# Kernel tuning notes

Measured on AMD Instinct MI355X. Metric: run time of the kernel, lower is better.

Reference implementation:

```python
import jax, jax.numpy as jnp
import numpy as np

B, S, C, D, P = 32, 720, 2048, 256, 96
LATENT_DIMS = [512, 128, 32]  # enc_in // 4 ** k, e_layers=3
NL = 3
ALPHA = 0.1
EPS = 1e-5


def _ln(x, g, b, eps=1e-5):
    m = jnp.mean(x, axis=-1, keepdims=True)
    v = jnp.var(x, axis=-1, keepdims=True)
    return (x - m) * jax.lax.rsqrt(v + eps) * g + b


def _cov_loss(skips, lam=ALPHA, eps=EPS):
    total = jnp.zeros((), dtype=jnp.float32)
    for x in skips[1:]:
        b, c, d = x.shape
        xr = x.reshape(b * c, d)
        xc = (xr - jnp.mean(xr, axis=0, keepdims=True)) / (jnp.std(xr, axis=0, ddof=1, keepdims=True) + eps)
        cov = xc.T @ xc / (b * c - 1) + eps * jnp.eye(d, dtype=x.dtype)
        total = total - jnp.linalg.slogdet(cov)[1] / d
    return lam * total / (len(skips) - 1)


def setup_inputs() -> dict:
    key = jax.random.key(0)
    ks = jax.random.split(key, 16)
    w = lambda k, shp: (jax.random.normal(k, shp, dtype=jnp.float32) * 0.02)
    inp = {
        'x_enc': jax.random.normal(ks[0], (B, S, C), dtype=jnp.float32),
        'x_mark_enc': jnp.zeros((B, S, 4), dtype=jnp.float32),
        'x_dec': jnp.zeros((B, P, C), dtype=jnp.float32),
        'x_mark_dec': jnp.zeros((B, P, 4), dtype=jnp.float32),
        'in_w': w(ks[1], (S, D)), 'in_b': jnp.zeros((D,), jnp.float32),
        'lq0': jax.random.normal(ks[2], (LATENT_DIMS[0], D), dtype=jnp.float32),
        'lq1': jax.random.normal(ks[3], (LATENT_DIMS[1], D), dtype=jnp.float32),
        'lq2': jax.random.normal(ks[4], (LATENT_DIMS[2], D), dtype=jnp.float32),
        'down_w': w(ks[5], (NL, 4, D, D)), 'down_b': jnp.zeros((NL, 4, D), jnp.float32),
        'down_ln': jnp.stack([jnp.ones((NL, D)), jnp.zeros((NL, D))], axis=1).astype(jnp.float32),
        'pred_w': w(ks[6], (D, D)), 'pred_b': jnp.zeros((D,), jnp.float32),
        'up_w': w(ks[7], (NL, 4, D, D)), 'up_b': jnp.zeros((NL, 4, D), jnp.float32),
        'up_ln': jnp.stack([jnp.ones((NL, D)), jnp.zeros((NL, D))], axis=1).astype(jnp.float32),
        'out_w': w(ks[8], (D, P)), 'out_b': jnp.zeros((P,), jnp.float32),
    }
    return inp


def _forward(x_enc, in_w, in_b, lqs, down_w, down_b, down_ln,
             pred_w, pred_b, up_w, up_b, up_ln, out_w, out_b):
    # instance norm over time
    means = jnp.mean(x_enc, axis=1, keepdims=True)            # [B,1,C]
    xc = x_enc - means
    stdev = jnp.sqrt(jnp.var(xc, axis=1, keepdims=True) + 1e-5)
    xn = xc / stdev
    # transpose + Linear(seq_len -> d_model): [B,C,D]
    h = jnp.einsum('bsc,sd->bcd', xn, in_w) + in_b

    scale = 1.0 / jnp.sqrt(jnp.asarray(D, dtype=h.dtype))
    skips = [h]
    x = h
    for i in range(NL):
        Wq, Wk, Wv, Wo = down_w[i]
        bq, bk, bv, bo = down_b[i]
        q = lqs[i] @ Wq + bq                                  # [Lq,D] shared over batch
        k = x @ Wk + bk                                       # [B,L,D]
        v = x @ Wv + bv
        attn = jax.nn.softmax(jnp.einsum('qd,bld->bql', q, k) * scale, axis=-1)
        o = jnp.einsum('bql,bld->bqd', attn, v) @ Wo + bo
        x = _ln(o, down_ln[i, 0], down_ln[i, 1])
        skips.append(x)

    cov = _cov_loss(skips)

    x = x @ pred_w + pred_b                                   # bottom [B,32,D]
    queries = skips[::-1][1:]                                 # [128-skip, 512-skip, base]
    for i, qin in enumerate(queries):
        Wq, Wk, Wv, Wo = up_w[i]
        bq, bk, bv, bo = up_b[i]
        q = qin @ Wq + bq                                     # [B,Lq,D]
        k = x @ Wk + bk                                       # [B,Lk,D]
        v = x @ Wv + bv
        attn = jax.nn.softmax(jnp.einsum('bqd,bld->bql', q, k) * scale, axis=-1)
        o = jnp.einsum('bql,bld->bqd', attn, v) @ Wo + bo
        x = _ln(o + qin, up_ln[i, 0], up_ln[i, 1])

    dec = (x + h) @ out_w + out_b                             # [B,C,P]
    dec = jnp.transpose(dec, (0, 2, 1))                       # [B,P,C]
    dec = dec * stdev[:, 0, :][:, None, :] + means[:, 0, :][:, None, :]
    return dec, cov


def reference(x_enc, x_mark_enc, x_dec, x_mark_dec, in_w, in_b, lq0, lq1, lq2,
              down_w, down_b, down_ln, pred_w, pred_b, up_w, up_b, up_ln, out_w, out_b):
    return _forward(x_enc, in_w, in_b, (lq0, lq1, lq2), down_w, down_b, down_ln,
                    pred_w, pred_b, up_w, up_b, up_ln, out_w, out_b)
```

## Files before the change

kernel.cpp:

```cpp
#include <hip/hip_runtime.h>
#include <hip/hip_bf16.h>
#include <math.h>

#define CDIV(a, b) (((a) + (b) - 1) / (b))
typedef long long ll;
typedef unsigned short ushort_t;

constexpr int Bn = 32;
constexpr int Sn = 720;
constexpr int SnP = 736;
constexpr int Cn = 2048;
constexpr int Dn = 256;
constexpr int Pn = 96;

typedef __attribute__((ext_vector_type(8))) short bf16x8;
typedef __attribute__((ext_vector_type(4))) float f32x4;

__device__ inline ushort_t rne1(float x) {
  unsigned u = __float_as_uint(x);
  u = (u + 0x7fffu + ((u >> 16) & 1u)) >> 16;
  return (ushort_t)u;
}
__device__ inline float b2f(ushort_t u) { return __uint_as_float(((unsigned)u) << 16); }

__device__ inline void gl_lds16(const void* g, void* l) {
  __builtin_amdgcn_global_load_lds(
      (const __attribute__((address_space(1))) void*)g,
      (__attribute__((address_space(3))) void*)l, 16, 0, 0);
}

__global__ void instnorm_stats(const float* __restrict__ x,
                               float* __restrict__ mean, float* __restrict__ stdev) {
  int c = blockIdx.x * 256 + threadIdx.x;
  int b = blockIdx.y;
  const float* p = x + (ll)b * Sn * Cn + c;
  float s = 0.f, q = 0.f;
  for (int t = 0; t < Sn; ++t) {
    float v = p[(ll)t * Cn];
    s += v; q += v * v;
  }
  float m = s / (float)Sn;
  float var = q / (float)Sn - m * m;
  var = fmaxf(var, 0.f);
  mean[b * Cn + c] = m;
  stdev[b * Cn + c] = sqrtf(var + 1e-5f);
}

__global__ void normT_kernel(const float* __restrict__ X, ushort_t* __restrict__ D,
                             const float* __restrict__ mean,
                             const float* __restrict__ stdev) {
  int b = blockIdx.z;
  __shared__ float tl[32][33];
  int t = threadIdx.x;
  int tx = t & 31, ty = t >> 5;
  int s0 = blockIdx.y * 32, c0 = blockIdx.x * 32;
#pragma unroll
  for (int e = 0; e < 4; ++e) {
    int s = s0 + ty + 8 * e;
    tl[ty + 8 * e][tx] = (s < Sn) ? X[((ll)b * Sn + s) * Cn + c0 + tx] : 0.f;
  }
  __syncthreads();
#pragma unroll
  for (int e = 0; e < 4; ++e) {
    int c = c0 + ty + 8 * e, s = s0 + tx;
    if (s < SnP) {
      float mu = mean[b * Cn + c], sd = stdev[b * Cn + c];
      float v = (s < Sn) ? (tl[tx][ty + 8 * e] - mu) / sd : 0.f;
      D[((ll)b * Cn + c) * SnP + s] = rne1(v);
    }
  }
}

__global__ void cvtT_kernel(const float* __restrict__ S, ushort_t* __restrict__ D,
                            int K, int N, int KP) {
  int z = blockIdx.z;
  S += (ll)z * K * N;
  D += (ll)z * N * KP;
  __shared__ float tl[32][33];
  int t = threadIdx.x;
  int tx = t & 31, ty = t >> 5;
  int k0 = blockIdx.y * 32, n0 = blockIdx.x * 32;
#pragma unroll
  for (int e = 0; e < 4; ++e) {
    int k = k0 + ty + 8 * e;
    tl[ty + 8 * e][tx] = (k < K && n0 + tx < N) ? S[(ll)k * N + n0 + tx] : 0.f;
  }
  __syncthreads();
#pragma unroll
  for (int e = 0; e < 4; ++e) {
    int n = n0 + ty + 8 * e, kk = k0 + tx;
    if (n < N && kk < KP) D[(ll)n * KP + kk] = rne1(tl[tx][ty + 8 * e]);
  }
}

__global__ void cvt_bf(const float* __restrict__ S, ushort_t* __restrict__ D, int n) {
  int i = blockIdx.x * 256 + threadIdx.x;
  if (i < n) D[i] = rne1(S[i]);
}

template <int MODE>
__global__ __launch_bounds__(256) void gemm_bf(
    const ushort_t* __restrict__ A, const ushort_t* __restrict__ B,
    int M, int N, int K, int lda, int ldb, ll sA, ll sB,
    const float* __restrict__ bias, float alpha,
    float* __restrict__ Cf, int ldcf, ll sCf,
    ushort_t* __restrict__ Cb, int ldcb, ll sCb) {
  int g = blockIdx.z;
  A += (ll)g * sA;
  B += (ll)g * sB;
  if (MODE & 1) Cf += (ll)g * sCf;
  if (MODE & 6) Cb += (ll)g * sCb;
  __shared__ ushort_t lds_ab[2][128][32];
  int t = threadIdx.x;
  int m0 = blockIdx.y * 128, n0 = blockIdx.x * 128;
  int w = t >> 6, lane = t & 63;
  int wm = (w >> 1) * 64, wn = (w & 1) * 64;
  int lrow = lane & 15, kq = lane >> 4;
  int srow = lane >> 2, skcol = (lane & 3) * 8;
  f32x4 acc[4][4] = {};
  for (int k0 = 0; k0 < K; k0 += 32) {
#pragma unroll
    for (int cc = 0; cc < 4; ++cc) {
      int c = w * 4 + cc;
      int tile = c >> 3, rb = (c & 7) * 16;
      int row = rb + srow;
      const ushort_t* src;
      if (tile == 0) {
        int gm = min(m0 + row, M - 1);
        src = &A[(ll)gm * lda + k0 + skcol];
      } else {
        int gn = min(n0 + row, N - 1);
        src = &B[(ll)gn * ldb + k0 + skcol];
      }
      gl_lds16(src, &lds_ab[tile][rb][0]);
    }
    __syncthreads();
    bf16x8 af[4], bfr[4];
#pragma unroll
    for (int i = 0; i < 4; ++i)
      af[i] = *reinterpret_cast<const bf16x8*>(&lds_ab[0][wm + i * 16 + lrow][kq * 8]);
#pragma unroll
    for (int j = 0; j < 4; ++j)
      bfr[j] = *reinterpret_cast<const bf16x8*>(&lds_ab[1][wn + j * 16 + lrow][kq * 8]);
#pragma unroll
    for (int i = 0; i < 4; ++i)
#pragma unroll
      for (int j = 0; j < 4; ++j)
        acc[i][j] = __builtin_amdgcn_mfma_f32_16x16x32_bf16(af[i], bfr[j],
                                                            acc[i][j], 0, 0, 0);
    __syncthreads();
  }
#pragma unroll
  for (int i = 0; i < 4; ++i) {
    int mb = m0 + wm + i * 16 + kq * 4;
    if (mb >= M) continue;
#pragma unroll
    for (int j = 0; j < 4; ++j) {
      int c = n0 + wn + j * 16 + lrow;
      if (c >= N) continue;
      float bv = bias ? bias[c] : 0.f;
#pragma unroll
      for (int reg = 0; reg < 4; ++reg) {
        int m = mb + reg;
        float v = acc[i][j][reg] * alpha + bv;
        if (MODE & 1) Cf[(ll)m * ldcf + c] = v;
        if (MODE & 2) Cb[(ll)m * ldcb + c] = rne1(v);
        if (MODE & 4) Cb[(ll)c * ldcb + m] = rne1(v);
      }
    }
  }
}

__device__ inline float blk_reduce(float v, volatile float* sh, int op) {
  int lane = threadIdx.x & 63, w = threadIdx.x >> 6;
#pragma unroll
  for (int off = 32; off > 0; off >>= 1) {
    float o = __shfl_down(v, off, 64);
    v = op ? fmaxf(v, o) : (v + o);
  }
  __syncthreads();
  if (lane == 0) sh[w] = v;
  __syncthreads();
  float r = op ? fmaxf(fmaxf(sh[0], sh[1]), fmaxf(sh[2], sh[3]))
               : (sh[0] + sh[1] + sh[2] + sh[3]);
  return r;
}

template <int LL>
__global__ void softmax_bf(const float* __restrict__ S, ushort_t* __restrict__ P) {
  constexpr int NE = (LL + 255) / 256;
  __shared__ float sh[4];
  ll row = blockIdx.x;
  const float* p = S + row * (ll)LL;
  ushort_t* q = P + row * (ll)LL;
  int t = threadIdx.x;
  float e[NE];
  float mx = -INFINITY;
#pragma unroll
  for (int k = 0; k < NE; ++k) {
    int i = t + k * 256;
    if (i < LL) { e[k] = p[i]; mx = fmaxf(mx, e[k]); }
  }
  mx = blk_reduce(mx, sh, 1);
  float sum = 0.f;
#pragma unroll
  for (int k = 0; k < NE; ++k) {
    int i = t + k * 256;
    if (i < LL) { e[k] = __expf(e[k] - mx); sum += e[k]; }
  }
  sum = blk_reduce(sum, sh, 0);
  float inv = 1.f / sum;
#pragma unroll
  for (int k = 0; k < NE; ++k) {
    int i = t + k * 256;
    if (i < LL) q[i] = rne1(e[k] * inv);
  }
}

__global__ void ln_kernel(const float* __restrict__ X, const ushort_t* __restrict__ RESb,
                          float* __restrict__ Yf, ushort_t* __restrict__ Yb, int postadd,
                          const float* __restrict__ gamma, const float* __restrict__ beta) {
  __shared__ float sh[4];
  ll row = blockIdx.x;
  int t = threadIdx.x;
  float r = RESb ? b2f(RESb[row * Dn + t]) : 0.f;
  float v = X[row * Dn + t] + r;
  float m = blk_reduce(v, sh, 0) * (1.f / (float)Dn);
  float d = v - m;
  float var = blk_reduce(d * d, sh, 0) * (1.f / (float)Dn);
  float y = d * rsqrtf(var + 1e-5f) * gamma[t] + beta[t];
  if (Yf) Yf[row * Dn + t] = y;
  if (Yb) Yb[row * Dn + t] = rne1(y + (postadd ? r : 0.f));
}

__global__ void colstat_partial(const float* __restrict__ X, double* __restrict__ part,
                                int nrows) {
  int blk = blockIdx.x, t = threadIdx.x;
  int chunk = CDIV(nrows, 256);
  int r0 = blk * chunk, r1 = min(nrows, r0 + chunk);
  double s = 0.0, q = 0.0;
  for (int r = r0; r < r1; ++r) {
    double v = (double)X[(ll)r * Dn + t];
    s += v; q += v * v;
  }
  part[blk * 512 + t] = s;
  part[blk * 512 + 256 + t] = q;
}

__global__ void colstat_final(const double* __restrict__ part, float* __restrict__ cmean,
                              float* __restrict__ cistd, int nrows) {
  int t = threadIdx.x;
  double s = 0.0, q = 0.0;
  for (int b = 0; b < 256; ++b) {
    s += part[b * 512 + t];
    q += part[b * 512 + 256 + t];
  }
  double m = s / (double)nrows;
  double var = (q - (double)nrows * m * m) / (double)(nrows - 1);
  var = fmax(var, 0.0);
  cmean[t] = (float)m;
  cistd[t] = (float)(1.0 / (sqrt(var) + 1e-5));
}

__global__ void xcnorm_kernel(const float* __restrict__ X, float* __restrict__ XC,
                              const float* __restrict__ cmean,
                              const float* __restrict__ cistd, ll n) {
  for (ll i = blockIdx.x * 256LL + threadIdx.x; i < n; i += (ll)gridDim.x * 256) {
    int d = (int)(i & 255);
    XC[i] = (X[i] - cmean[d]) * cistd[d];
  }
}

__global__ __launch_bounds__(256) void cov_gemm_f64_split(const float* __restrict__ XC,
                                                          double* __restrict__ part,
                                                          int nr) {
  __shared__ float Am[32][33];
  __shared__ float Bq[32][33];
  int t = threadIdx.x;
  int tx = t & 31, ty = t >> 5;
  int m0 = blockIdx.y * 32, n0 = blockIdx.x * 32;
  int z = blockIdx.z;
  int chunk = nr >> 4;
  int kbeg = z * chunk, kend = kbeg + chunk;
  double acc[4] = {0.0, 0.0, 0.0, 0.0};
  for (int k0 = kbeg; k0 < kend; k0 += 32) {
#pragma unroll
    for (int e = 0; e < 4; ++e) {
      int idx = t + e * 256;
      int kk = idx >> 5, mm = idx & 31;
      Am[kk][mm] = XC[(ll)(k0 + kk) * Dn + m0 + mm];
      Bq[kk][mm] = XC[(ll)(k0 + kk) * Dn + n0 + mm];
    }
    __syncthreads();
#pragma unroll 8
    for (int kk = 0; kk < 32; ++kk) {
      float bv = Bq[kk][tx];
#pragma unroll
      for (int r = 0; r < 4; ++r)
        acc[r] += (double)Am[kk][ty + 8 * r] * (double)bv;
    }
    __syncthreads();
  }
#pragma unroll
  for (int r = 0; r < 4; ++r) {
    int m = m0 + ty + 8 * r, n = n0 + tx;
    part[(ll)z * 65536 + m * 256 + n] = acc[r];
  }
}

__global__ void cov_reduce(const double* __restrict__ part, double* __restrict__ Cd,
                           double inv) {
  int idx = blockIdx.x * 256 + threadIdx.x;
  double s = 0.0;
#pragma unroll
  for (int z = 0; z < 16; ++z) s += part[(ll)z * 65536 + idx];
  int m = idx >> 8, n = idx & 255;
  Cd[idx] = s * inv + ((m == n) ? 1e-5 : 0.0);
}

__global__ __launch_bounds__(256) void chol_step_a(double* __restrict__ mats, int d0) {
  double* A = mats + (ll)blockIdx.x * 65536;
  __shared__ double D[32][33];
  __shared__ double dinv[32];
  int t = threadIdx.x;
  for (int e = t; e < 1024; e += 256)
    D[e >> 5][e & 31] = A[(ll)(d0 + (e >> 5)) * 256 + d0 + (e & 31)];
  __syncthreads();
  if (t < 32) {
    double x[32];
#pragma unroll
    for (int j = 0; j < 32; ++j) x[j] = D[t][j];
#pragma unroll
    for (int k = 0; k < 32; ++k) {
      double piv = fmax(__shfl(x[k], k, 64), 1e-300);
      double inv = 1.0 / sqrt(piv);
      double lrk = x[k] * inv;
      x[k] = lrk;
#pragma unroll
      for (int j = k + 1; j < 32; ++j) x[j] -= lrk * __shfl(lrk, j, 64);
    }
#pragma unroll
    for (int j = 0; j < 32; ++j) D[t][j] = x[j];
    dinv[t] = 1.0 / x[t];
  }
  __syncthreads();
  int r = d0 + 32 + t;
  if (r < 256) {
    double y[32];
#pragma unroll
    for (int j = 0; j < 32; ++j) y[j] = A[(ll)r * 256 + d0 + j];
#pragma unroll
    for (int j = 0; j < 32; ++j) {
      double s = y[j];
#pragma unroll
      for (int i = 0; i < j; ++i) s -= y[i] * D[j][i];
      y[j] = s * dinv[j];
    }
#pragma unroll
    for (int j = 0; j < 32; ++j) A[(ll)r * 256 + d0 + j] = y[j];
  }
  for (int e = t; e < 1024; e += 256)
    A[(ll)(d0 + (e >> 5)) * 256 + d0 + (e & 31)] = D[e >> 5][e & 31];
}

__global__ __launch_bounds__(256) void chol_step_b(double* __restrict__ mats, int d0) {
  double* A = mats + (ll)blockIdx.y * 65536;
  int tile = blockIdx.x;
  int i = 0;
  while (tile >= i + 1) { tile -= i + 1; ++i; }
  int j = tile;
  int ri = d0 + 32 + i * 32, rj = d0 + 32 + j * 32;
  __shared__ double Li[32][33];
  __shared__ double Lj[32][33];
  int t = threadIdx.x;
  for (int e = t; e < 1024; e += 256) {
    int rr = e >> 5, kk = e & 31;
    Li[rr][kk] = A[(ll)(ri + rr) * 256 + d0 + kk];
    Lj[rr][kk] = A[(ll)(rj + rr) * 256 + d0 + kk];
  }
  __syncthreads();
  for (int e = t; e < 1024; e += 256) {
    int rr = e >> 5, cc = e & 31;
    double s = 0.0;
#pragma unroll
    for (int k = 0; k < 32; ++k) s += Li[rr][k] * Lj[cc][k];
    A[(ll)(ri + rr) * 256 + rj + cc] -= s;
  }
}

__global__ void logdet_diag(const double* __restrict__ mats, double* __restrict__ ld) {
  __shared__ double sh[4];
  const double* A = mats + (ll)blockIdx.x * 65536;
  int t = threadIdx.x;
  double lg = log(A[(ll)t * 257]);
  int lane = t & 63, w = t >> 6;
#pragma unroll
  for (int off = 32; off > 0; off >>= 1) lg += __shfl_down(lg, off, 64);
  if (lane == 0) sh[w] = lg;
  __syncthreads();
  if (t == 0) ld[blockIdx.x] = 2.0 * (sh[0] + sh[1] + sh[2] + sh[3]);
}

__global__ void cov_final(const double* __restrict__ ld, float* __restrict__ outp) {
  outp[0] = (float)(-0.1 / (3.0 * 256.0) * (ld[0] + ld[1] + ld[2]));
}

__global__ __launch_bounds__(256) void out_mfma(
    const ushort_t* __restrict__ A, const ushort_t* __restrict__ B,
    const float* __restrict__ bias, const float* __restrict__ stdev,
    const float* __restrict__ mean, float* __restrict__ out) {
  constexpr int M = Bn * Cn, N = Pn, K = Dn;
  __shared__ ushort_t lds_ab[2][128][32];
  int t = threadIdx.x;
  int m0 = blockIdx.y * 128;
  int w = t >> 6, lane = t & 63;
  int wm = (w >> 1) * 64, wn = (w & 1) * 64;
  int lrow = lane & 15, kq = lane >> 4;
  int srow = lane >> 2, skcol = (lane & 3) * 8;
  f32x4 acc[4][4] = {};
  for (int k0 = 0; k0 < K; k0 += 32) {
#pragma unroll
    for (int cc = 0; cc < 4; ++cc) {
      int c = w * 4 + cc;
      int tile = c >> 3, rb = (c & 7) * 16;
      int row = rb + srow;
      const ushort_t* src;
      if (tile == 0) {
        src = &A[(ll)(m0 + row) * K + k0 + skcol];
      } else {
        int gn = min(row, N - 1);
        src = &B[(ll)gn * K + k0 + skcol];
      }
      gl_lds16(src, &lds_ab[tile][rb][0]);
    }
    __syncthreads();
    bf16x8 af[4], bfr[4];
#pragma unroll
    for (int i = 0; i < 4; ++i)
      af[i] = *reinterpret_cast<const bf16x8*>(&lds_ab[0][wm + i * 16 + lrow][kq * 8]);
#pragma unroll
    for (int j = 0; j < 4; ++j)
      bfr[j] = *reinterpret_cast<const bf16x8*>(&lds_ab[1][wn + j * 16 + lrow][kq * 8]);
#pragma unroll
    for (int i = 0; i < 4; ++i)
#pragma unroll
      for (int j = 0; j < 4; ++j)
        acc[i][j] = __builtin_amdgcn_mfma_f32_16x16x32_bf16(af[i], bfr[j],
                                                            acc[i][j], 0, 0, 0);
    __syncthreads();
  }
#pragma unroll
  for (int i = 0; i < 4; ++i) {
    int mb = m0 + wm + i * 16 + kq * 4;
#pragma unroll
    for (int j = 0; j < 4; ++j) {
      int p = wn + j * 16 + lrow;
      if (p >= N) continue;
      float bv = bias[p];
#pragma unroll
      for (int reg = 0; reg < 4; ++reg) {
        int m = mb + reg;
        int b = m >> 11, c = m & 2047;
        float v = acc[i][j][reg] + bv;
        out[((ll)(b * Pn + p)) * Cn + c] = v * stdev[m] + mean[m];
      }
    }
  }
}

extern "C" void kernel_launch(void* const* d_in, const int* in_sizes, int n_in,
                              void* d_out, int out_size, void* d_ws, size_t ws_size,
                              hipStream_t stream) {
  (void)in_sizes; (void)n_in; (void)out_size; (void)ws_size;
  const float* x_enc = (const float*)d_in[0];
  const float* in_w = (const float*)d_in[4];
  const float* in_b = (const float*)d_in[5];
  const float* lq[3] = {(const float*)d_in[6], (const float*)d_in[7],
                        (const float*)d_in[8]};
  const float* down_w = (const float*)d_in[9];
  const float* down_b = (const float*)d_in[10];
  const float* down_ln = (const float*)d_in[11];
  const float* pred_w = (const float*)d_in[12];
  const float* pred_b = (const float*)d_in[13];
  const float* up_w = (const float*)d_in[14];
  const float* up_b = (const float*)d_in[15];
  const float* up_ln = (const float*)d_in[16];
  const float* out_w = (const float*)d_in[17];
  const float* out_b = (const float*)d_in[18];
  float* out = (float*)d_out;

  float* ws = (float*)d_ws;
  size_t off = 0;
  auto alloc = [&](size_t n) {
    n = (n + 3) & ~(size_t)3;
    float* p = ws + off;
    off += n;
    return p;
  };
  float* mean = alloc((size_t)Bn * Cn);
  float* stdevv = alloc((size_t)Bn * Cn);
  float* cmean = alloc(256);
  float* cistd = alloc(256);
  double* part = (double*)alloc(256 * 512 * 2);
  double* ld = (double*)alloc(16);
  double* covd = (double*)alloc(3 * 65536 * 2);
  float* s1 = alloc((size_t)Bn * 512 * Dn);
  float* s2 = alloc((size_t)Bn * 128 * Dn);
  float* s3 = alloc((size_t)Bn * 32 * Dn);
  float* attn = alloc((size_t)Bn * 512 * 2048);
  float* sbuf = alloc((size_t)16777216);
  ushort_t* h_bf = (ushort_t*)alloc((size_t)Bn * Cn * Dn / 2);
  ushort_t* s1b = (ushort_t*)alloc((size_t)Bn * 512 * Dn / 2);
  ushort_t* s2b = (ushort_t*)alloc((size_t)Bn * 128 * Dn / 2);
  ushort_t* s3b = (ushort_t*)alloc((size_t)Bn * 32 * Dn / 2);
  ushort_t* xpb = (ushort_t*)alloc((size_t)Bn * 32 * Dn / 2);
  ushort_t* xu0b = (ushort_t*)alloc((size_t)Bn * 128 * Dn / 2);
  ushort_t* xu1b = (ushort_t*)alloc((size_t)Bn * 512 * Dn / 2);
  ushort_t* qd_b = (ushort_t*)alloc(512 * 256 / 2);
  ushort_t* lqb0 = (ushort_t*)alloc(512 * 256 / 2);
  ushort_t* lqb1 = (ushort_t*)alloc(128 * 256 / 2);
  ushort_t* lqb2 = (ushort_t*)alloc(32 * 256 / 2);
  ushort_t* in_wT = (ushort_t*)alloc(256 * SnP / 2);
  ushort_t* downT = (ushort_t*)alloc(12 * 65536 / 2);
  ushort_t* upT = (ushort_t*)alloc(12 * 65536 / 2);
  ushort_t* predT = (ushort_t*)alloc(65536 / 2);
  ushort_t* outT = (ushort_t*)alloc(96 * 256 / 2);
  ushort_t* q_bf = (ushort_t*)alloc((size_t)Bn * 2048 * Dn / 2);
  ushort_t* k_bf = (ushort_t*)alloc((size_t)Bn * 2048 * Dn / 2);
  ushort_t* vT = (ushort_t*)alloc((size_t)Bn * 2048 * Dn / 2);

  ushort_t* xnT = (ushort_t*)attn;
  ushort_t* attn_b = (ushort_t*)sbuf;
  float* o2 = sbuf;
  double* covpart = (double*)sbuf;
  const float scale = 0.0625f;
  const float* npf = nullptr;

  instnorm_stats<<<dim3(Cn / 256, Bn), 256, 0, stream>>>(x_enc, mean, stdevv);
  normT_kernel<<<dim3(Cn / 32, SnP / 32, Bn), 256, 0, stream>>>(x_enc, xnT, mean,
                                                                stdevv);
  cvtT_kernel<<<dim3(8, 8, 12), 256, 0, stream>>>(down_w, downT, 256, 256, 256);
  cvtT_kernel<<<dim3(8, 8, 12), 256, 0, stream>>>(up_w, upT, 256, 256, 256);
  cvtT_kernel<<<dim3(8, 8, 1), 256, 0, stream>>>(pred_w, predT, 256, 256, 256);
  cvtT_kernel<<<dim3(8, SnP / 32, 1), 256, 0, stream>>>(in_w, in_wT, Sn, 256, SnP);
  cvtT_kernel<<<dim3(3, 8, 1), 256, 0, stream>>>(out_w, outT, 256, Pn, 256);
  cvt_bf<<<512, 256, 0, stream>>>(lq[0], lqb0, 512 * 256);
  cvt_bf<<<128, 256, 0, stream>>>(lq[1], lqb1, 128 * 256);
  cvt_bf<<<32, 256, 0, stream>>>(lq[2], lqb2, 32 * 256);

  gemm_bf<2><<<dim3(2, 16, Bn), 256, 0, stream>>>(
      xnT, in_wT, Cn, Dn, SnP, SnP, SnP, (ll)Cn * SnP, 0, in_b, 1.f,
      nullptr, 0, 0, h_bf, Dn, (ll)Cn * Dn);

  ushort_t* lqb[3] = {lqb0, lqb1, lqb2};
  float* skf[3] = {s1, s2, s3};
  ushort_t* skb[3] = {s1b, s2b, s3b};
  int Ls[4] = {2048, 512, 128, 32};
  const ushort_t* xinb = h_bf;

  for (int i = 0; i < 3; ++i) {
    int L = Ls[i], Lq = Ls[i + 1];
    const ushort_t* WqT = downT + (size_t)(i * 4 + 0) * 65536;
    const ushort_t* WkT = downT + (size_t)(i * 4 + 1) * 65536;
    const ushort_t* WvT = downT + (size_t)(i * 4 + 2) * 65536;
    const ushort_t* WoT = downT + (size_t)(i * 4 + 3) * 65536;
    const float* bq = down_b + (i * 4 + 0) * 256;
    const float* bk = down_b + (i * 4 + 1) * 256;
    const float* bv = down_b + (i * 4 + 2) * 256;
    const float* bo = down_b + (i * 4 + 3) * 256;

    gemm_bf<2><<<dim3(2, CDIV(Lq, 128), 1), 256, 0, stream>>>(
        lqb[i], WqT, Lq, Dn, Dn, Dn, Dn, 0, 0, bq, 1.f, nullptr, 0, 0, qd_b, Dn, 0);
    gemm_bf<2><<<dim3(2, (Bn * L) / 128, 1), 256, 0, stream>>>(
        xinb, WkT, Bn * L, Dn, Dn, Dn, Dn, 0, 0, bk, 1.f, nullptr, 0, 0, k_bf, Dn, 0);
    gemm_bf<4><<<dim3(2, L / 128, Bn), 256, 0, stream>>>(
        xinb, WvT, L, Dn, Dn, Dn, Dn, (ll)L * Dn, 0, bv, 1.f, nullptr, 0, 0,
        vT, L, (ll)Dn * L);
    gemm_bf<1><<<dim3(L / 128, CDIV(Lq, 128), Bn), 256, 0, stream>>>(
        qd_b, k_bf, Lq, L, Dn, Dn, Dn, 0, (ll)L * Dn, npf, scale,
        attn, L, (ll)Lq * L, nullptr, 0, 0);
    if (L == 2048) softmax_bf<2048><<<Bn * Lq, 256, 0, stream>>>(attn, attn_b);
    else if (L == 512) softmax_bf<512><<<Bn * Lq, 256, 0, stream>>>(attn, attn_b);
    else softmax_bf<128><<<Bn * Lq, 256, 0, stream>>>(attn, attn_b);
    gemm_bf<2><<<dim3(2, CDIV(Lq, 128), Bn), 256, 0, stream>>>(
        attn_b, vT, Lq, Dn, L, L, L, (ll)Lq * L, (ll)Dn * L, npf, 1.f,
        nullptr, 0, 0, q_bf, Dn, (ll)Lq * Dn);
    gemm_bf<1><<<dim3(2, CDIV(Bn * Lq, 128), 1), 256, 0, stream>>>(
        q_bf, WoT, Bn * Lq, Dn, Dn, Dn, Dn, 0, 0, bo, 1.f, o2, Dn, 0, nullptr, 0, 0);
    ln_kernel<<<Bn * Lq, 256, 0, stream>>>(o2, nullptr, skf[i], skb[i], 0,
                                           down_ln + (i * 2 + 0) * 256,
                                           down_ln + (i * 2 + 1) * 256);
    xinb = skb[i];
  }

  int nrs[3] = {Bn * 512, Bn * 128, Bn * 32};
  float* xc = attn;
  for (int j = 0; j < 3; ++j) {
    int nr = nrs[j];
    colstat_partial<<<256, 256, 0, stream>>>(skf[j], part, nr);
    colstat_final<<<1, 256, 0, stream>>>(part, cmean, cistd, nr);
    xcnorm_kernel<<<1024, 256, 0, stream>>>(skf[j], xc, cmean, cistd, (ll)nr * Dn);
    cov_gemm_f64_split<<<dim3(8, 8, 16), 256, 0, stream>>>(xc, covpart, nr);
    cov_reduce<<<256, 256, 0, stream>>>(covpart, covd + (size_t)j * 65536,
                                        1.0 / (double)(nr - 1));
  }
  for (int kb = 0; kb < 8; ++kb) {
    chol_step_a<<<3, 256, 0, stream>>>(covd, kb * 32);
    int T = 7 - kb;
    if (T > 0)
      chol_step_b<<<dim3(T * (T + 1) / 2, 3), 256, 0, stream>>>(covd, kb * 32);
  }
  logdet_diag<<<3, 256, 0, stream>>>(covd, ld);
  cov_final<<<1, 1, 0, stream>>>(ld, out + 6291456);

  gemm_bf<2><<<dim3(2, 8, 1), 256, 0, stream>>>(
      s3b, predT, Bn * 32, Dn, Dn, Dn, Dn, 0, 0, pred_b, 1.f,
      nullptr, 0, 0, xpb, Dn, 0);

  int Lks[3] = {32, 128, 512}, Lqs[3] = {128, 512, 2048};
  const ushort_t* qinb[3] = {s2b, s1b, h_bf};
  const ushort_t* xinbs[3] = {xpb, xu0b, xu1b};
  ushort_t* xoutb[3] = {xu0b, xu1b, q_bf};
  for (int i = 0; i < 3; ++i) {
    int Lk = Lks[i], Lq = Lqs[i];
    const ushort_t* WqT = upT + (size_t)(i * 4 + 0) * 65536;
    const ushort_t* WkT = upT + (size_t)(i * 4 + 1) * 65536;
    const ushort_t* WvT = upT + (size_t)(i * 4 + 2) * 65536;
    const ushort_t* WoT = upT + (size_t)(i * 4 + 3) * 65536;
    const float* bq = up_b + (i * 4 + 0) * 256;
    const float* bk = up_b + (i * 4 + 1) * 256;
    const float* bv = up_b + (i * 4 + 2) * 256;
    const float* bo = up_b + (i * 4 + 3) * 256;

    gemm_bf<2><<<dim3(2, (Bn * Lq) / 128, 1), 256, 0, stream>>>(
        qinb[i], WqT, Bn * Lq, Dn, Dn, Dn, Dn, 0, 0, bq, 1.f,
        nullptr, 0, 0, q_bf, Dn, 0);
    gemm_bf<2><<<dim3(2, CDIV(Bn * Lk, 128), 1), 256, 0, stream>>>(
        xinbs[i], WkT, Bn * Lk, Dn, Dn, Dn, Dn, 0, 0, bk, 1.f,
        nullptr, 0, 0, k_bf, Dn, 0);
    gemm_bf<4><<<dim3(2, CDIV(Lk, 128), Bn), 256, 0, stream>>>(
        xinbs[i], WvT, Lk, Dn, Dn, Dn, Dn, (ll)Lk * Dn, 0, bv, 1.f,
        nullptr, 0, 0, vT, Lk, (ll)Dn * Lk);
    gemm_bf<1><<<dim3(CDIV(Lk, 128), CDIV(Lq, 128), Bn), 256, 0, stream>>>(
        q_bf, k_bf, Lq, Lk, Dn, Dn, Dn, (ll)Lq * Dn, (ll)Lk * Dn, npf, scale,
        attn, Lk, (ll)Lq * Lk, nullptr, 0, 0);
    if (Lk == 32) softmax_bf<32><<<Bn * Lq, 256, 0, stream>>>(attn, attn_b);
    else if (Lk == 128) softmax_bf<128><<<Bn * Lq, 256, 0, stream>>>(attn, attn_b);
    else softmax_bf<512><<<Bn * Lq, 256, 0, stream>>>(attn, attn_b);
    gemm_bf<2><<<dim3(2, CDIV(Lq, 128), Bn), 256, 0, stream>>>(
        attn_b, vT, Lq, Dn, Lk, Lk, Lk, (ll)Lq * Lk, (ll)Dn * Lk, npf, 1.f,
        nullptr, 0, 0, q_bf, Dn, (ll)Lq * Dn);
    gemm_bf<1><<<dim3(2, (Bn * Lq) / 128, 1), 256, 0, stream>>>(
        q_bf, WoT, Bn * Lq, Dn, Dn, Dn, Dn, 0, 0, bo, 1.f, o2, Dn, 0, nullptr, 0, 0);
    ln_kernel<<<Bn * Lq, 256, 0, stream>>>(o2, qinb[i], nullptr, xoutb[i],
                                           (i == 2) ? 1 : 0,
                                           up_ln + (i * 2 + 0) * 256,
                                           up_ln + (i * 2 + 1) * 256);
  }

  out_mfma<<<dim3(1, (Bn * Cn) / 128, 1), 256, 0, stream>>>(q_bf, outT, out_b,
                                                            stdevv, mean, out);
}
```

Before: 1.856 ms.

## Fuse column normalization into covariance Gram kernel and compute only lower triangle

New measurement: 1.854 ms. No clear change (-0.1%).

```diff
diff --git a/kernel.cpp b/kernel.cpp
--- a/kernel.cpp
+++ b/kernel.cpp
@@ -262,24 +262,25 @@
   cistd[t] = (float)(1.0 / (sqrt(var) + 1e-5));
 }
 
-__global__ void xcnorm_kernel(const float* __restrict__ X, float* __restrict__ XC,
-                              const float* __restrict__ cmean,
-                              const float* __restrict__ cistd, ll n) {
-  for (ll i = blockIdx.x * 256LL + threadIdx.x; i < n; i += (ll)gridDim.x * 256) {
-    int d = (int)(i & 255);
-    XC[i] = (X[i] - cmean[d]) * cistd[d];
-  }
-}
-
-__global__ __launch_bounds__(256) void cov_gemm_f64_split(const float* __restrict__ XC,
-                                                          double* __restrict__ part,
-                                                          int nr) {
-  __shared__ float Am[32][33];
-  __shared__ float Bq[32][33];
-  int t = threadIdx.x;
-  int tx = t & 31, ty = t >> 5;
-  int m0 = blockIdx.y * 32, n0 = blockIdx.x * 32;
-  int z = blockIdx.z;
+__global__ __launch_bounds__(256) void cov_gram(const float* __restrict__ X,
+                                                const float* __restrict__ cmean,
+                                                const float* __restrict__ cistd,
+                                                double* __restrict__ part, int nr) {
+  __shared__ double Am[32][33];
+  __shared__ double Bq[32][33];
+  __shared__ float cmA[32], ciA[32], cmB[32], ciB[32];
+  int tile = blockIdx.x;
+  int mi = 0;
+  while (tile >= mi + 1) { tile -= mi + 1; ++mi; }
+  int nj = tile;
+  int m0 = mi * 32, n0 = nj * 32;
+  int z = blockIdx.y;
+  int t = threadIdx.x, tx = t & 31, ty = t >> 5;
+  if (t < 32) {
+    cmA[t] = cmean[m0 + t]; ciA[t] = cistd[m0 + t];
+    cmB[t] = cmean[n0 + t]; ciB[t] = cistd[n0 + t];
+  }
+  __syncthreads();
   int chunk = nr >> 4;
   int kbeg = z * chunk, kend = kbeg + chunk;
   double acc[4] = {0.0, 0.0, 0.0, 0.0};
@@ -288,16 +289,18 @@
     for (int e = 0; e < 4; ++e) {
       int idx = t + e * 256;
       int kk = idx >> 5, mm = idx & 31;
-      Am[kk][mm] = XC[(ll)(k0 + kk) * Dn + m0 + mm];
-      Bq[kk][mm] = XC[(ll)(k0 + kk) * Dn + n0 + mm];
+      float xa = X[(ll)(k0 + kk) * Dn + m0 + mm];
+      float xb = X[(ll)(k0 + kk) * Dn + n0 + mm];
+      Am[kk][mm] = (double)((xa - cmA[mm]) * ciA[mm]);
+      Bq[kk][mm] = (double)((xb - cmB[mm]) * ciB[mm]);
     }
     __syncthreads();
 #pragma unroll 8
     for (int kk = 0; kk < 32; ++kk) {
-      float bv = Bq[kk][tx];
+      double bv = Bq[kk][tx];
 #pragma unroll
       for (int r = 0; r < 4; ++r)
-        acc[r] += (double)Am[kk][ty + 8 * r] * (double)bv;
+        acc[r] += Am[kk][ty + 8 * r] * bv;
     }
     __syncthreads();
   }
@@ -310,12 +313,22 @@
 
 __global__ void cov_reduce(const double* __restrict__ part, double* __restrict__ Cd,
                            double inv) {
-  int idx = blockIdx.x * 256 + threadIdx.x;
-  double s = 0.0;
-#pragma unroll
-  for (int z = 0; z < 16; ++z) s += part[(ll)z * 65536 + idx];
-  int m = idx >> 8, n = idx & 255;
-  Cd[idx] = s * inv + ((m == n) ? 1e-5 : 0.0);
+  int tile = blockIdx.x;
+  int mi = 0;
+  while (tile >= mi + 1) { tile -= mi + 1; ++mi; }
+  int nj = tile;
+  int t = threadIdx.x;
+#pragma unroll
+  for (int e = 0; e < 4; ++e) {
+    int idx = t + e * 256;
+    int rr = idx >> 5, cc = idx & 31;
+    int m = mi * 32 + rr, n = nj * 32 + cc;
+    int off = m * 256 + n;
+    double s = 0.0;
+#pragma unroll
+    for (int z = 0; z < 16; ++z) s += part[(ll)z * 65536 + off];
+    Cd[off] = s * inv + ((m == n) ? 1e-5 : 0.0);
+  }
 }
 
 __global__ __launch_bounds__(256) void chol_step_a(double* __restrict__ mats, int d0) {
@@ -323,8 +336,10 @@
   __shared__ double D[32][33];
   __shared__ double dinv[32];
   int t = threadIdx.x;
-  for (int e = t; e < 1024; e += 256)
-    D[e >> 5][e & 31] = A[(ll)(d0 + (e >> 5)) * 256 + d0 + (e & 31)];
+  for (int e = t; e < 1024; e += 256) {
+    int i = e >> 5, j = e & 31;
+    D[i][j] = (j <= i) ? A[(ll)(d0 + i) * 256 + d0 + j] : 0.0;
+  }
   __syncthreads();
   if (t < 32) {
     double x[32];
@@ -594,15 +609,13 @@
   }
 
   int nrs[3] = {Bn * 512, Bn * 128, Bn * 32};
-  float* xc = attn;
   for (int j = 0; j < 3; ++j) {
     int nr = nrs[j];
     colstat_partial<<<256, 256, 0, stream>>>(skf[j], part, nr);
     colstat_final<<<1, 256, 0, stream>>>(part, cmean, cistd, nr);
-    xcnorm_kernel<<<1024, 256, 0, stream>>>(skf[j], xc, cmean, cistd, (ll)nr * Dn);
-    cov_gemm_f64_split<<<dim3(8, 8, 16), 256, 0, stream>>>(xc, covpart, nr);
-    cov_reduce<<<256, 256, 0, stream>>>(covpart, covd + (size_t)j * 65536,
-                                        1.0 / (double)(nr - 1));
+    cov_gram<<<dim3(36, 16), 256, 0, stream>>>(skf[j], cmean, cistd, covpart, nr);
+    cov_reduce<<<36, 256, 0, stream>>>(covpart, covd + (size_t)j * 65536,
+                                       1.0 / (double)(nr - 1));
   }
   for (int kb = 0; kb < 8; ++kb) {
     chol_step_a<<<3, 256, 0, stream>>>(covd, kb * 32);
```
